# Kernel tuning notes

Hardware: AMD Instinct MI355X
Metric: run time of the kernel (lower is better)

## Reference

```python
import jax, jax.numpy as jnp
import numpy as np

NUM_GROUPS = 256   # number of distinct gt instance ids per image
EPS = 1e-6
PULL_W = 1.0
PUSH_W = 1.0
LOSS_W = 1.0


def setup_inputs() -> dict:
    key = jax.random.key(0)
    k1, k2, k3 = jax.random.split(key, 3)
    B, N, D = 16, 16384, 256
    pred = jax.random.normal(k1, (B, N, D), dtype=jnp.float32)
    gt_inds = jax.random.randint(k2, (B, N), 0, NUM_GROUPS, dtype=jnp.int32)
    anchor_inds = jax.random.randint(k3, (B, N), 0, 9, dtype=jnp.int32)
    return {"pred": pred, "gt_inds": gt_inds, "anchor_inds": anchor_inds}


def _single_image_loss(p, g):
    # p: [N, D] tag embeddings, g: [N] int group ids in [0, NUM_GROUPS)
    ones = jnp.ones(g.shape, dtype=p.dtype)
    counts = jax.ops.segment_sum(ones, g, num_segments=NUM_GROUPS)          # [G]
    sums = jax.ops.segment_sum(p, g, num_segments=NUM_GROUPS)               # [G, D]
    tags = sums / jnp.maximum(counts, 1.0)[:, None]                         # group means

    # pull: per-element cosine to own group's tag (torch cos eps clamp on norm product)
    tag_per = tags[g]                                                       # [N, D]
    dot = jnp.sum(p * tag_per, axis=1)
    denom = jnp.maximum(jnp.linalg.norm(p, axis=1) * jnp.linalg.norm(tag_per, axis=1), EPS)
    one_minus_cos = 1.0 - dot / denom                                       # [N]
    pull_g = jax.ops.segment_sum(one_minus_cos, g, num_segments=NUM_GROUPS) / jnp.maximum(counts, 1.0)

    present = counts > 0
    obj_num = jnp.sum(present.astype(p.dtype))
    pull = jnp.sum(jnp.where(present, pull_g, 0.0)) / (obj_num + EPS)

    # push: pairwise cosine over group tags (incl. diagonal, then subtract 2*obj_num)
    tn = jnp.linalg.norm(tags, axis=1)                                      # [G]
    cosmat = (tags @ tags.T) / jnp.maximum(tn[:, None] * tn[None, :], EPS)  # [G, G]
    pair_mask = present[:, None] & present[None, :]
    push_sum = jnp.sum(jnp.where(pair_mask, 1.0 + cosmat, 0.0)) - 2.0 * obj_num
    push = push_sum / (((obj_num - 1.0) * obj_num + EPS) * 2.0)

    loss = PUSH_W * push + PULL_W * pull
    # original returns 0 when only a single group exists
    return jnp.where(obj_num > 1.0, loss, 0.0)


def reference(pred, gt_inds, anchor_inds):
    per_img = jax.vmap(_single_image_loss)(pred, gt_inds)   # [B]
    return LOSS_W * jnp.mean(per_img)
```

## Files before the change

kernel.cpp:

```cpp
#include <hip/hip_runtime.h>

#define B_ 16
#define N_ 16384
#define D_ 256
#define G_ 256
#define EPSF 1e-6f

template <int CTRL>
__device__ __forceinline__ float dpp_add_step(float x) {
    const int y = __builtin_amdgcn_update_dpp(0, __float_as_int(x), CTRL, 0xF, 0xF, false);
    return x + __int_as_float(y);
}
__device__ __forceinline__ float wave_sum64(float x) {
    x = dpp_add_step<0x111>(x);
    x = dpp_add_step<0x112>(x);
    x = dpp_add_step<0x114>(x);
    x = dpp_add_step<0x118>(x);
    x = dpp_add_step<0x142>(x);
    x = dpp_add_step<0x143>(x);
    return __int_as_float(__builtin_amdgcn_readlane(__float_as_int(x), 63));
}

__global__ __launch_bounds__(1024) void k_sort(const int* __restrict__ gt,
                                               int* __restrict__ counts,
                                               int* __restrict__ starts,
                                               int* __restrict__ sorted) {
    __shared__ int hist[G_];
    __shared__ int scn[G_];
    const int tid = threadIdx.x, b = blockIdx.x;
    if (tid < G_) hist[tid] = 0;
    __syncthreads();
    const int base = b * N_;
    #pragma unroll
    for (int k = 0; k < N_/1024; ++k)
        atomicAdd(&hist[gt[base + k*1024 + tid]], 1);
    __syncthreads();
    int c = 0;
    if (tid < G_) {
        c = hist[tid];
        counts[b*G_ + tid] = c;
        scn[tid] = c;
    }
    __syncthreads();
    for (int off = 1; off < G_; off <<= 1) {
        int v = 0;
        if (tid < G_ && tid >= off) v = scn[tid - off];
        __syncthreads();
        if (tid < G_) scn[tid] += v;
        __syncthreads();
    }
    if (tid < G_) {
        const int st = scn[tid] - c;
        starts[b*G_ + tid] = st;
        hist[tid] = st;
    }
    __syncthreads();
    #pragma unroll
    for (int k = 0; k < N_/1024; ++k) {
        const int r = k*1024 + tid;
        const int g = gt[base + r];
        const int pos = atomicAdd(&hist[g], 1);
        sorted[base + pos] = r;
    }
}

__global__ __launch_bounds__(256, 5) void k_fused(const float* __restrict__ pred,
                                                  const int* __restrict__ sorted,
                                                  const int* __restrict__ starts,
                                                  const int* __restrict__ counts,
                                                  float* __restrict__ sums,
                                                  float* __restrict__ pull_g) {
    const int tid = threadIdx.x, lane = tid & 63, w = tid >> 6;
    const int gi = (blockIdx.x << 2) | w;
    const int b = gi >> 8;
    const int start = starts[gi], cnt = counts[gi];
    const int c = lane * 4;

    if (cnt == 0) {
        float4 z = make_float4(0.f,0.f,0.f,0.f);
        *(float4*)&sums[(size_t)gi*D_ + c] = z;
        if (lane == 0) pull_g[gi] = 0.f;
        return;
    }

    const float* predb = pred + (size_t)b*N_*D_;
    const int*   sortb = sorted + b*N_ + start;

    float4 acc  = make_float4(0.f,0.f,0.f,0.f);
    float4 uacc = make_float4(0.f,0.f,0.f,0.f);
    int i = 0;

    if (cnt <= 128) {
        const int ids0 = sortb[min(lane, cnt-1)];
        int ids1 = 0;
        if (cnt > 64) ids1 = sortb[min(64 + lane, cnt-1)];
        #define GET2(k) (((k) < 64) ? __builtin_amdgcn_readlane(ids0, (k)) \
                                    : __builtin_amdgcn_readlane(ids1, (k) - 64))
        for (; i + 8 <= cnt; i += 8) {
            const int r0 = GET2(i+0), r1 = GET2(i+1), r2 = GET2(i+2), r3 = GET2(i+3);
            const int r4 = GET2(i+4), r5 = GET2(i+5), r6 = GET2(i+6), r7 = GET2(i+7);
            const float4 p0 = *(const float4*)&predb[(size_t)r0*D_ + c];
            const float4 p1 = *(const float4*)&predb[(size_t)r1*D_ + c];
            const float4 p2 = *(const float4*)&predb[(size_t)r2*D_ + c];
            const float4 p3 = *(const float4*)&predb[(size_t)r3*D_ + c];
            const float4 p4 = *(const float4*)&predb[(size_t)r4*D_ + c];
            const float4 p5 = *(const float4*)&predb[(size_t)r5*D_ + c];
            const float4 p6 = *(const float4*)&predb[(size_t)r6*D_ + c];
            const float4 p7 = *(const float4*)&predb[(size_t)r7*D_ + c];
            float n0 = p0.x*p0.x + p0.y*p0.y + p0.z*p0.z + p0.w*p0.w;
            float n1 = p1.x*p1.x + p1.y*p1.y + p1.z*p1.z + p1.w*p1.w;
            float n2 = p2.x*p2.x + p2.y*p2.y + p2.z*p2.z + p2.w*p2.w;
            float n3 = p3.x*p3.x + p3.y*p3.y + p3.z*p3.z + p3.w*p3.w;
            float n4 = p4.x*p4.x + p4.y*p4.y + p4.z*p4.z + p4.w*p4.w;
            float n5 = p5.x*p5.x + p5.y*p5.y + p5.z*p5.z + p5.w*p5.w;
            float n6 = p6.x*p6.x + p6.y*p6.y + p6.z*p6.z + p6.w*p6.w;
            float n7 = p7.x*p7.x + p7.y*p7.y + p7.z*p7.z + p7.w*p7.w;
            n0 = wave_sum64(n0); n1 = wave_sum64(n1);
            n2 = wave_sum64(n2); n3 = wave_sum64(n3);
            n4 = wave_sum64(n4); n5 = wave_sum64(n5);
            n6 = wave_sum64(n6); n7 = wave_sum64(n7);
            const float q0 = __frsqrt_rn(n0), q1 = __frsqrt_rn(n1);
            const float q2 = __frsqrt_rn(n2), q3 = __frsqrt_rn(n3);
            const float q4 = __frsqrt_rn(n4), q5 = __frsqrt_rn(n5);
            const float q6 = __frsqrt_rn(n6), q7 = __frsqrt_rn(n7);
            acc.x  += ((p0.x + p1.x) + (p2.x + p3.x)) + ((p4.x + p5.x) + (p6.x + p7.x));
            acc.y  += ((p0.y + p1.y) + (p2.y + p3.y)) + ((p4.y + p5.y) + (p6.y + p7.y));
            acc.z  += ((p0.z + p1.z) + (p2.z + p3.z)) + ((p4.z + p5.z) + (p6.z + p7.z));
            acc.w  += ((p0.w + p1.w) + (p2.w + p3.w)) + ((p4.w + p5.w) + (p6.w + p7.w));
            uacc.x += ((p0.x*q0 + p1.x*q1) + (p2.x*q2 + p3.x*q3)) + ((p4.x*q4 + p5.x*q5) + (p6.x*q6 + p7.x*q7));
            uacc.y += ((p0.y*q0 + p1.y*q1) + (p2.y*q2 + p3.y*q3)) + ((p4.y*q4 + p5.y*q5) + (p6.y*q6 + p7.y*q7));
            uacc.z += ((p0.z*q0 + p1.z*q1) + (p2.z*q2 + p3.z*q3)) + ((p4.z*q4 + p5.z*q5) + (p6.z*q6 + p7.z*q7));
            uacc.w += ((p0.w*q0 + p1.w*q1) + (p2.w*q2 + p3.w*q3)) + ((p4.w*q4 + p5.w*q5) + (p6.w*q6 + p7.w*q7));
        }
        for (; i < cnt; ++i) {
            const int r0 = GET2(i);
            const float4 p0 = *(const float4*)&predb[(size_t)r0*D_ + c];
            const float n0 = wave_sum64(p0.x*p0.x + p0.y*p0.y + p0.z*p0.z + p0.w*p0.w);
            const float q0 = __frsqrt_rn(n0);
            acc.x  += p0.x;    acc.y  += p0.y;    acc.z  += p0.z;    acc.w  += p0.w;
            uacc.x += p0.x*q0; uacc.y += p0.y*q0; uacc.z += p0.z*q0; uacc.w += p0.w*q0;
        }
        #undef GET2
    } else {
        for (; i < cnt; ++i) {
            const int r0 = sortb[i];
            const float4 p0 = *(const float4*)&predb[(size_t)r0*D_ + c];
            const float n0 = wave_sum64(p0.x*p0.x + p0.y*p0.y + p0.z*p0.z + p0.w*p0.w);
            const float q0 = __frsqrt_rn(n0);
            acc.x  += p0.x;    acc.y  += p0.y;    acc.z  += p0.z;    acc.w  += p0.w;
            uacc.x += p0.x*q0; uacc.y += p0.y*q0; uacc.z += p0.z*q0; uacc.w += p0.w*q0;
        }
    }

    *(float4*)&sums[(size_t)gi*D_ + c] = acc;

    const float ssq = wave_sum64(acc.x*acc.x + acc.y*acc.y + acc.z*acc.z + acc.w*acc.w);
    const float dus = wave_sum64(uacc.x*acc.x + uacc.y*acc.y + uacc.z*acc.z + uacc.w*acc.w);
    if (lane == 0) pull_g[gi] = (float)cnt - dus / sqrtf(ssq);
}

__global__ __launch_bounds__(256) void k_tags(const float* __restrict__ sums,
                                              const int* __restrict__ counts,
                                              const float* __restrict__ pull_g,
                                              float* __restrict__ lossv) {
    const int b = blockIdx.x;
    const int tid = threadIdx.x;
    const int lane = tid & 63;
    const int wave = tid >> 6;
    __shared__ float s_acc[D_];
    __shared__ float redA[256];
    __shared__ float redB[256];

    for (int i = tid; i < D_; i += 256) s_acc[i] = 0.f;
    __syncthreads();

    const int c = lane * 4;
    float4 sl = make_float4(0.f, 0.f, 0.f, 0.f);
    for (int g = wave; g < G_; g += 4) {
        const int cnt = counts[b*G_ + g];
        const float inv = 1.0f / fmaxf((float)cnt, 1.0f);
        const float4 sm = *(const float4*)&sums[((size_t)(b*G_ + g))*D_ + c];
        const float tx = sm.x*inv, tyv = sm.y*inv, tz = sm.z*inv, tw = sm.w*inv;
        const float sq = wave_sum64(tx*tx + tyv*tyv + tz*tz + tw*tw);
        if (cnt > 0) {
            const float it = __frsqrt_rn(sq);
            sl.x += tx*it; sl.y += tyv*it; sl.z += tz*it; sl.w += tw*it;
        }
    }
    atomicAdd(&s_acc[c+0], sl.x);
    atomicAdd(&s_acc[c+1], sl.y);
    atomicAdd(&s_acc[c+2], sl.z);
    atomicAdd(&s_acc[c+3], sl.w);
    __syncthreads();

    const int cnt_t = counts[b*G_ + tid];
    const float v = s_acc[tid];
    redA[tid] = v * v;
    redB[tid] = (cnt_t > 0) ? 1.f : 0.f;
    __syncthreads();
    for (int s = 128; s > 0; s >>= 1) {
        if (tid < s) { redA[tid] += redA[tid + s]; redB[tid] += redB[tid + s]; }
        __syncthreads();
    }
    float ssq = 0.f, obj = 0.f;
    if (tid == 0) { ssq = redA[0]; obj = redB[0]; }
    __syncthreads();

    redA[tid] = (cnt_t > 0) ? pull_g[b*G_ + tid] / (float)cnt_t : 0.f;
    __syncthreads();
    for (int s = 128; s > 0; s >>= 1) {
        if (tid < s) redA[tid] += redA[tid + s];
        __syncthreads();
    }
    if (tid == 0) {
        const float push = (obj*obj - 2.f*obj + ssq) / (((obj - 1.f)*obj + EPSF) * 2.f);
        const float pull = redA[0] / (obj + EPSF);
        lossv[b] = (obj > 1.f) ? (push + pull) : 0.f;
    }
}

__global__ void k_out(const float* __restrict__ lossv, float* __restrict__ out) {
    if (threadIdx.x == 0) {
        float t = 0.f;
        #pragma unroll
        for (int b = 0; b < B_; ++b) t += lossv[b];
        out[0] = t * (1.0f / (float)B_);
    }
}

extern "C" void kernel_launch(void* const* d_in, const int* in_sizes, int n_in,
                              void* d_out, int out_size, void* d_ws, size_t ws_size,
                              hipStream_t stream) {
    const float* pred = (const float*)d_in[0];
    const int*   gt   = (const int*)d_in[1];
    float* out = (float*)d_out;

    char* ws = (char*)d_ws;
    const size_t SZ_SUMS = (size_t)B_*G_*D_*sizeof(float);
    const size_t SZ_I    = (size_t)B_*G_*sizeof(int);

    float* sums    = (float*)ws;                               ws += SZ_SUMS;
    int*   counts  = (int*)ws;                                 ws += SZ_I;
    int*   starts  = (int*)ws;                                 ws += SZ_I;
    float* pull_g  = (float*)ws;                               ws += SZ_I;
    float* lossv   = (float*)ws;                               ws += 64*sizeof(float);
    int*   sorted  = (int*)ws;

    k_sort  <<<B_,        1024, 0, stream>>>(gt, counts, starts, sorted);
    k_fused <<<B_*G_/4,    256, 0, stream>>>(pred, sorted, starts, counts, sums, pull_g);
    k_tags  <<<B_,         256, 0, stream>>>(sums, counts, pull_g, lossv);
    k_out   <<<1,           64, 0, stream>>>(lossv, out);
}
```

Baseline: 95.75 us.

## Fuse tag/loss reduction into main kernel via last-block atomics; use 16-bit sort indices

Removes the separate k_tags and k_out launches. Each block bumps a per-image counter, and the last block for an image computes that image's push/pull loss. A second counter lets the final image's block write the mean output. The sorted index array also shrinks to unsigned short, which halves its traffic. This saves two launch gaps at the cost of atomics, fences and a serialized tail in the last block per image.

Result: slower. 175.2 us (+83.0%).

```diff
diff --git a/kernel.cpp b/kernel.cpp
--- a/kernel.cpp
+++ b/kernel.cpp
@@ -5,6 +5,8 @@
 #define D_ 256
 #define G_ 256
 #define EPSF 1e-6f
+
+#define DEV_LDF(p) __hip_atomic_load((p), __ATOMIC_RELAXED, __HIP_MEMORY_SCOPE_AGENT)
 
 template <int CTRL>
 __device__ __forceinline__ float dpp_add_step(float x) {
@@ -24,10 +26,12 @@
 __global__ __launch_bounds__(1024) void k_sort(const int* __restrict__ gt,
                                                int* __restrict__ counts,
                                                int* __restrict__ starts,
-                                               int* __restrict__ sorted) {
+                                               unsigned short* __restrict__ sorted,
+                                               int* __restrict__ done) {
     __shared__ int hist[G_];
     __shared__ int scn[G_];
     const int tid = threadIdx.x, b = blockIdx.x;
+    if (b == 0 && tid < 17) done[tid] = 0;
     if (tid < G_) hist[tid] = 0;
     __syncthreads();
     const int base = b * N_;
@@ -60,16 +64,19 @@
         const int r = k*1024 + tid;
         const int g = gt[base + r];
         const int pos = atomicAdd(&hist[g], 1);
-        sorted[base + pos] = r;
+        sorted[base + pos] = (unsigned short)r;
     }
 }
 
 __global__ __launch_bounds__(256, 5) void k_fused(const float* __restrict__ pred,
-                                                  const int* __restrict__ sorted,
+                                                  const unsigned short* __restrict__ sorted,
                                                   const int* __restrict__ starts,
                                                   const int* __restrict__ counts,
                                                   float* __restrict__ sums,
-                                                  float* __restrict__ pull_g) {
+                                                  float* __restrict__ pull_g,
+                                                  int* __restrict__ done,
+                                                  float* __restrict__ lossv,
+                                                  float* __restrict__ out) {
     const int tid = threadIdx.x, lane = tid & 63, w = tid >> 6;
     const int gi = (blockIdx.x << 2) | w;
     const int b = gi >> 8;
@@ -80,111 +87,110 @@
         float4 z = make_float4(0.f,0.f,0.f,0.f);
         *(float4*)&sums[(size_t)gi*D_ + c] = z;
         if (lane == 0) pull_g[gi] = 0.f;
-        return;
-    }
-
-    const float* predb = pred + (size_t)b*N_*D_;
-    const int*   sortb = sorted + b*N_ + start;
-
-    float4 acc  = make_float4(0.f,0.f,0.f,0.f);
-    float4 uacc = make_float4(0.f,0.f,0.f,0.f);
-    int i = 0;
-
-    if (cnt <= 128) {
-        const int ids0 = sortb[min(lane, cnt-1)];
-        int ids1 = 0;
-        if (cnt > 64) ids1 = sortb[min(64 + lane, cnt-1)];
-        #define GET2(k) (((k) < 64) ? __builtin_amdgcn_readlane(ids0, (k)) \
-                                    : __builtin_amdgcn_readlane(ids1, (k) - 64))
-        for (; i + 8 <= cnt; i += 8) {
-            const int r0 = GET2(i+0), r1 = GET2(i+1), r2 = GET2(i+2), r3 = GET2(i+3);
-            const int r4 = GET2(i+4), r5 = GET2(i+5), r6 = GET2(i+6), r7 = GET2(i+7);
-            const float4 p0 = *(const float4*)&predb[(size_t)r0*D_ + c];
-            const float4 p1 = *(const float4*)&predb[(size_t)r1*D_ + c];
-            const float4 p2 = *(const float4*)&predb[(size_t)r2*D_ + c];
-            const float4 p3 = *(const float4*)&predb[(size_t)r3*D_ + c];
-            const float4 p4 = *(const float4*)&predb[(size_t)r4*D_ + c];
-            const float4 p5 = *(const float4*)&predb[(size_t)r5*D_ + c];
-            const float4 p6 = *(const float4*)&predb[(size_t)r6*D_ + c];
-            const float4 p7 = *(const float4*)&predb[(size_t)r7*D_ + c];
-            float n0 = p0.x*p0.x + p0.y*p0.y + p0.z*p0.z + p0.w*p0.w;
-            float n1 = p1.x*p1.x + p1.y*p1.y + p1.z*p1.z + p1.w*p1.w;
-            float n2 = p2.x*p2.x + p2.y*p2.y + p2.z*p2.z + p2.w*p2.w;
-            float n3 = p3.x*p3.x + p3.y*p3.y + p3.z*p3.z + p3.w*p3.w;
-            float n4 = p4.x*p4.x + p4.y*p4.y + p4.z*p4.z + p4.w*p4.w;
-            float n5 = p5.x*p5.x + p5.y*p5.y + p5.z*p5.z + p5.w*p5.w;
-            float n6 = p6.x*p6.x + p6.y*p6.y + p6.z*p6.z + p6.w*p6.w;
-            float n7 = p7.x*p7.x + p7.y*p7.y + p7.z*p7.z + p7.w*p7.w;
-            n0 = wave_sum64(n0); n1 = wave_sum64(n1);
-            n2 = wave_sum64(n2); n3 = wave_sum64(n3);
-            n4 = wave_sum64(n4); n5 = wave_sum64(n5);
-            n6 = wave_sum64(n6); n7 = wave_sum64(n7);
-            const float q0 = __frsqrt_rn(n0), q1 = __frsqrt_rn(n1);
-            const float q2 = __frsqrt_rn(n2), q3 = __frsqrt_rn(n3);
-            const float q4 = __frsqrt_rn(n4), q5 = __frsqrt_rn(n5);
-            const float q6 = __frsqrt_rn(n6), q7 = __frsqrt_rn(n7);
-            acc.x  += ((p0.x + p1.x) + (p2.x + p3.x)) + ((p4.x + p5.x) + (p6.x + p7.x));
-            acc.y  += ((p0.y + p1.y) + (p2.y + p3.y)) + ((p4.y + p5.y) + (p6.y + p7.y));
-            acc.z  += ((p0.z + p1.z) + (p2.z + p3.z)) + ((p4.z + p5.z) + (p6.z + p7.z));
-            acc.w  += ((p0.w + p1.w) + (p2.w + p3.w)) + ((p4.w + p5.w) + (p6.w + p7.w));
-            uacc.x += ((p0.x*q0 + p1.x*q1) + (p2.x*q2 + p3.x*q3)) + ((p4.x*q4 + p5.x*q5) + (p6.x*q6 + p7.x*q7));
-            uacc.y += ((p0.y*q0 + p1.y*q1) + (p2.y*q2 + p3.y*q3)) + ((p4.y*q4 + p5.y*q5) + (p6.y*q6 + p7.y*q7));
-            uacc.z += ((p0.z*q0 + p1.z*q1) + (p2.z*q2 + p3.z*q3)) + ((p4.z*q4 + p5.z*q5) + (p6.z*q6 + p7.z*q7));
-            uacc.w += ((p0.w*q0 + p1.w*q1) + (p2.w*q2 + p3.w*q3)) + ((p4.w*q4 + p5.w*q5) + (p6.w*q6 + p7.w*q7));
+    } else {
+        const float* predb = pred + (size_t)b*N_*D_;
+        const unsigned short* sortb = sorted + b*N_ + start;
+
+        float4 acc  = make_float4(0.f,0.f,0.f,0.f);
+        float4 uacc = make_float4(0.f,0.f,0.f,0.f);
+        int i = 0;
+
+        if (cnt <= 128) {
+            const int ids0 = (int)sortb[min(lane, cnt-1)];
+            int ids1 = 0;
+            if (cnt > 64) ids1 = (int)sortb[min(64 + lane, cnt-1)];
+            #define GET2(k) (((k) < 64) ? __builtin_amdgcn_readlane(ids0, (k)) \
+                                        : __builtin_amdgcn_readlane(ids1, (k) - 64))
+            for (; i + 8 <= cnt; i += 8) {
+                const int r0 = GET2(i+0), r1 = GET2(i+1), r2 = GET2(i+2), r3 = GET2(i+3);
+                const int r4 = GET2(i+4), r5 = GET2(i+5), r6 = GET2(i+6), r7 = GET2(i+7);
+                const float4 p0 = *(const float4*)&predb[(size_t)r0*D_ + c];
+                const float4 p1 = *(const float4*)&predb[(size_t)r1*D_ + c];
+                const float4 p2 = *(const float4*)&predb[(size_t)r2*D_ + c];
+                const float4 p3 = *(const float4*)&predb[(size_t)r3*D_ + c];
+                const float4 p4 = *(const float4*)&predb[(size_t)r4*D_ + c];
+                const float4 p5 = *(const float4*)&predb[(size_t)r5*D_ + c];
+                const float4 p6 = *(const float4*)&predb[(size_t)r6*D_ + c];
+                const float4 p7 = *(const float4*)&predb[(size_t)r7*D_ + c];
+                float n0 = p0.x*p0.x + p0.y*p0.y + p0.z*p0.z + p0.w*p0.w;
+                float n1 = p1.x*p1.x + p1.y*p1.y + p1.z*p1.z + p1.w*p1.w;
+                float n2 = p2.x*p2.x + p2.y*p2.y + p2.z*p2.z + p2.w*p2.w;
+                float n3 = p3.x*p3.x + p3.y*p3.y + p3.z*p3.z + p3.w*p3.w;
+                float n4 = p4.x*p4.x + p4.y*p4.y + p4.z*p4.z + p4.w*p4.w;
+                float n5 = p5.x*p5.x + p5.y*p5.y + p5.z*p5.z + p5.w*p5.w;
+                float n6 = p6.x*p6.x + p6.y*p6.y + p6.z*p6.z + p6.w*p6.w;
+                float n7 = p7.x*p7.x + p7.y*p7.y + p7.z*p7.z + p7.w*p7.w;
+                n0 = wave_sum64(n0); n1 = wave_sum64(n1);
+                n2 = wave_sum64(n2); n3 = wave_sum64(n3);
+                n4 = wave_sum64(n4); n5 = wave_sum64(n5);
+                n6 = wave_sum64(n6); n7 = wave_sum64(n7);
+                const float q0 = __frsqrt_rn(n0), q1 = __frsqrt_rn(n1);
+                const float q2 = __frsqrt_rn(n2), q3 = __frsqrt_rn(n3);
+                const float q4 = __frsqrt_rn(n4), q5 = __frsqrt_rn(n5);
+                const float q6 = __frsqrt_rn(n6), q7 = __frsqrt_rn(n7);
+                acc.x  += ((p0.x + p1.x) + (p2.x + p3.x)) + ((p4.x + p5.x) + (p6.x + p7.x));
+                acc.y  += ((p0.y + p1.y) + (p2.y + p3.y)) + ((p4.y + p5.y) + (p6.y + p7.y));
+                acc.z  += ((p0.z + p1.z) + (p2.z + p3.z)) + ((p4.z + p5.z) + (p6.z + p7.z));
+                acc.w  += ((p0.w + p1.w) + (p2.w + p3.w)) + ((p4.w + p5.w) + (p6.w + p7.w));
+                uacc.x += ((p0.x*q0 + p1.x*q1) + (p2.x*q2 + p3.x*q3)) + ((p4.x*q4 + p5.x*q5) + (p6.x*q6 + p7.x*q7));
+                uacc.y += ((p0.y*q0 + p1.y*q1) + (p2.y*q2 + p3.y*q3)) + ((p4.y*q4 + p5.y*q5) + (p6.y*q6 + p7.y*q7));
+                uacc.z += ((p0.z*q0 + p1.z*q1) + (p2.z*q2 + p3.z*q3)) + ((p4.z*q4 + p5.z*q5) + (p6.z*q6 + p7.z*q7));
+                uacc.w += ((p0.w*q0 + p1.w*q1) + (p2.w*q2 + p3.w*q3)) + ((p4.w*q4 + p5.w*q5) + (p6.w*q6 + p7.w*q7));
+            }
+            for (; i < cnt; ++i) {
+                const int r0 = GET2(i);
+                const float4 p0 = *(const float4*)&predb[(size_t)r0*D_ + c];
+                const float n0 = wave_sum64(p0.x*p0.x + p0.y*p0.y + p0.z*p0.z + p0.w*p0.w);
+                const float q0 = __frsqrt_rn(n0);
+                acc.x  += p0.x;    acc.y  += p0.y;    acc.z  += p0.z;    acc.w  += p0.w;
+                uacc.x += p0.x*q0; uacc.y += p0.y*q0; uacc.z += p0.z*q0; uacc.w += p0.w*q0;
+            }
+            #undef GET2
+        } else {
+            for (; i < cnt; ++i) {
+                const int r0 = (int)sortb[i];
+                const float4 p0 = *(const float4*)&predb[(size_t)r0*D_ + c];
+                const float n0 = wave_sum64(p0.x*p0.x + p0.y*p0.y + p0.z*p0.z + p0.w*p0.w);
+                const float q0 = __frsqrt_rn(n0);
+                acc.x  += p0.x;    acc.y  += p0.y;    acc.z  += p0.z;    acc.w  += p0.w;
+                uacc.x += p0.x*q0; uacc.y += p0.y*q0; uacc.z += p0.z*q0; uacc.w += p0.w*q0;
+            }
         }
-        for (; i < cnt; ++i) {
-            const int r0 = GET2(i);
-            const float4 p0 = *(const float4*)&predb[(size_t)r0*D_ + c];
-            const float n0 = wave_sum64(p0.x*p0.x + p0.y*p0.y + p0.z*p0.z + p0.w*p0.w);
-            const float q0 = __frsqrt_rn(n0);
-            acc.x  += p0.x;    acc.y  += p0.y;    acc.z  += p0.z;    acc.w  += p0.w;
-            uacc.x += p0.x*q0; uacc.y += p0.y*q0; uacc.z += p0.z*q0; uacc.w += p0.w*q0;
-        }
-        #undef GET2
-    } else {
-        for (; i < cnt; ++i) {
-            const int r0 = sortb[i];
-            const float4 p0 = *(const float4*)&predb[(size_t)r0*D_ + c];
-            const float n0 = wave_sum64(p0.x*p0.x + p0.y*p0.y + p0.z*p0.z + p0.w*p0.w);
-            const float q0 = __frsqrt_rn(n0);
-            acc.x  += p0.x;    acc.y  += p0.y;    acc.z  += p0.z;    acc.w  += p0.w;
-            uacc.x += p0.x*q0; uacc.y += p0.y*q0; uacc.z += p0.z*q0; uacc.w += p0.w*q0;
-        }
-    }
-
-    *(float4*)&sums[(size_t)gi*D_ + c] = acc;
-
-    const float ssq = wave_sum64(acc.x*acc.x + acc.y*acc.y + acc.z*acc.z + acc.w*acc.w);
-    const float dus = wave_sum64(uacc.x*acc.x + uacc.y*acc.y + uacc.z*acc.z + uacc.w*acc.w);
-    if (lane == 0) pull_g[gi] = (float)cnt - dus / sqrtf(ssq);
-}
-
-__global__ __launch_bounds__(256) void k_tags(const float* __restrict__ sums,
-                                              const int* __restrict__ counts,
-                                              const float* __restrict__ pull_g,
-                                              float* __restrict__ lossv) {
-    const int b = blockIdx.x;
-    const int tid = threadIdx.x;
-    const int lane = tid & 63;
-    const int wave = tid >> 6;
+
+        *(float4*)&sums[(size_t)gi*D_ + c] = acc;
+        const float ssq = wave_sum64(acc.x*acc.x + acc.y*acc.y + acc.z*acc.z + acc.w*acc.w);
+        const float dus = wave_sum64(uacc.x*acc.x + uacc.y*acc.y + uacc.z*acc.z + uacc.w*acc.w);
+        if (lane == 0) pull_g[gi] = (float)cnt - dus / sqrtf(ssq);
+    }
+
+    __shared__ int islast;
+    __syncthreads();
+    if (tid == 0) {
+        __threadfence();
+        const int old = __hip_atomic_fetch_add(&done[b], 1, __ATOMIC_ACQ_REL,
+                                               __HIP_MEMORY_SCOPE_AGENT);
+        islast = (old == 63);
+    }
+    __syncthreads();
+    if (!islast) return;
+
     __shared__ float s_acc[D_];
     __shared__ float redA[256];
     __shared__ float redB[256];
-
-    for (int i = tid; i < D_; i += 256) s_acc[i] = 0.f;
-    __syncthreads();
-
-    const int c = lane * 4;
+    for (int i2 = tid; i2 < D_; i2 += 256) s_acc[i2] = 0.f;
+    __syncthreads();
+
     float4 sl = make_float4(0.f, 0.f, 0.f, 0.f);
-    for (int g = wave; g < G_; g += 4) {
-        const int cnt = counts[b*G_ + g];
-        const float inv = 1.0f / fmaxf((float)cnt, 1.0f);
-        const float4 sm = *(const float4*)&sums[((size_t)(b*G_ + g))*D_ + c];
-        const float tx = sm.x*inv, tyv = sm.y*inv, tz = sm.z*inv, tw = sm.w*inv;
-        const float sq = wave_sum64(tx*tx + tyv*tyv + tz*tz + tw*tw);
-        if (cnt > 0) {
+    for (int g = w; g < G_; g += 4) {
+        const int cg = counts[b*G_ + g];
+        const float inv = 1.0f / fmaxf((float)cg, 1.0f);
+        const float* smp = &sums[((size_t)(b*G_ + g))*D_ + c];
+        const float tx = DEV_LDF(smp+0)*inv, ty = DEV_LDF(smp+1)*inv;
+        const float tz = DEV_LDF(smp+2)*inv, tw = DEV_LDF(smp+3)*inv;
+        const float sq = wave_sum64(tx*tx + ty*ty + tz*tz + tw*tw);
+        if (cg > 0) {
             const float it = __frsqrt_rn(sq);
-            sl.x += tx*it; sl.y += tyv*it; sl.z += tz*it; sl.w += tw*it;
+            sl.x += tx*it; sl.y += ty*it; sl.z += tz*it; sl.w += tw*it;
         }
     }
     atomicAdd(&s_acc[c+0], sl.x);
@@ -202,29 +208,30 @@
         if (tid < s) { redA[tid] += redA[tid + s]; redB[tid] += redB[tid + s]; }
         __syncthreads();
     }
-    float ssq = 0.f, obj = 0.f;
-    if (tid == 0) { ssq = redA[0]; obj = redB[0]; }
-    __syncthreads();
-
-    redA[tid] = (cnt_t > 0) ? pull_g[b*G_ + tid] / (float)cnt_t : 0.f;
+    float ssq2 = 0.f, obj = 0.f;
+    if (tid == 0) { ssq2 = redA[0]; obj = redB[0]; }
+    __syncthreads();
+
+    redA[tid] = (cnt_t > 0) ? DEV_LDF(&pull_g[b*G_ + tid]) / (float)cnt_t : 0.f;
     __syncthreads();
     for (int s = 128; s > 0; s >>= 1) {
         if (tid < s) redA[tid] += redA[tid + s];
         __syncthreads();
     }
     if (tid == 0) {
-        const float push = (obj*obj - 2.f*obj + ssq) / (((obj - 1.f)*obj + EPSF) * 2.f);
+        const float push = (obj*obj - 2.f*obj + ssq2) / (((obj - 1.f)*obj + EPSF) * 2.f);
         const float pull = redA[0] / (obj + EPSF);
-        lossv[b] = (obj > 1.f) ? (push + pull) : 0.f;
-    }
-}
-
-__global__ void k_out(const float* __restrict__ lossv, float* __restrict__ out) {
-    if (threadIdx.x == 0) {
-        float t = 0.f;
-        #pragma unroll
-        for (int b = 0; b < B_; ++b) t += lossv[b];
-        out[0] = t * (1.0f / (float)B_);
+        const float loss = (obj > 1.f) ? (push + pull) : 0.f;
+        __hip_atomic_store(&lossv[b], loss, __ATOMIC_RELEASE, __HIP_MEMORY_SCOPE_AGENT);
+        const int o2 = __hip_atomic_fetch_add(&done[16], 1, __ATOMIC_ACQ_REL,
+                                              __HIP_MEMORY_SCOPE_AGENT);
+        if (o2 == 15) {
+            float t = 0.f;
+            #pragma unroll
+            for (int bb = 0; bb < B_; ++bb)
+                t += __hip_atomic_load(&lossv[bb], __ATOMIC_RELAXED, __HIP_MEMORY_SCOPE_AGENT);
+            out[0] = t * (1.0f / (float)B_);
+        }
     }
 }
 
@@ -244,10 +251,10 @@
     int*   starts  = (int*)ws;                                 ws += SZ_I;
     float* pull_g  = (float*)ws;                               ws += SZ_I;
     float* lossv   = (float*)ws;                               ws += 64*sizeof(float);
-    int*   sorted  = (int*)ws;
-
-    k_sort  <<<B_,        1024, 0, stream>>>(gt, counts, starts, sorted);
-    k_fused <<<B_*G_/4,    256, 0, stream>>>(pred, sorted, starts, counts, sums, pull_g);
-    k_tags  <<<B_,         256, 0, stream>>>(sums, counts, pull_g, lossv);
-    k_out   <<<1,           64, 0, stream>>>(lossv, out);
-}
+    int*   done    = (int*)ws;                                 ws += 64*sizeof(int);
+    unsigned short* sorted = (unsigned short*)ws;
+
+    k_sort  <<<B_,      1024, 0, stream>>>(gt, counts, starts, sorted, done);
+    k_fused <<<B_*G_/4,  256, 0, stream>>>(pred, sorted, starts, counts, sums,
+                                           pull_g, done, lossv, out);
+}
```
